# Kernel tuning notes

Hardware: AMD Instinct MI355X
Metric: run time of the kernel (lower is better)

## Reference

```python
import jax, jax.numpy as jnp
import numpy as np

D = 1024
H = 16
HD = D // H
FF = 4 * D
LN_EPS = 1e-5


def _layernorm(x, w, b):
    mu = jnp.mean(x, axis=-1, keepdims=True)
    var = jnp.mean(jnp.square(x - mu), axis=-1, keepdims=True)
    return (x - mu) * jax.lax.rsqrt(var + LN_EPS) * w + b


def setup_inputs() -> dict:
    key = jax.random.key(0)
    ks = jax.random.split(key, 12)
    s = 0.02
    return {
        "x": jax.random.normal(ks[0], (8, 1024, D), jnp.float32),
        "c": jax.random.normal(ks[1], (8, D), jnp.float32),
        "ln1_w": jnp.ones((D,), jnp.float32),
        "ln1_b": jnp.zeros((D,), jnp.float32),
        "ln2_w": jnp.ones((D,), jnp.float32),
        "ln2_b": jnp.zeros((D,), jnp.float32),
        "ada_w": jax.random.normal(ks[2], (D, 6 * D), jnp.float32) * s,
        "ada_b": jnp.zeros((6 * D,), jnp.float32),
        "qkv_w": jax.random.normal(ks[3], (D, 3 * D), jnp.float32) * s,
        "qkv_b": jnp.zeros((3 * D,), jnp.float32),
        "proj_w": jax.random.normal(ks[4], (D, D), jnp.float32) * s,
        "proj_b": jnp.zeros((D,), jnp.float32),
        "fc1_w": jax.random.normal(ks[5], (D, FF), jnp.float32) * s,
        "fc1_b": jnp.zeros((FF,), jnp.float32),
        "fc2_w": jax.random.normal(ks[6], (FF, D), jnp.float32) * s,
        "fc2_b": jnp.zeros((D,), jnp.float32),
    }


def reference(x, c, ln1_w, ln1_b, ln2_w, ln2_b, ada_w, ada_b,
              qkv_w, qkv_b, proj_w, proj_b, fc1_w, fc1_b, fc2_w, fc2_b):
    B, L, _ = x.shape
    # adaLN modulation: SiLU(c) @ W -> 6 chunks of (B, D)
    ssg = jax.nn.silu(c) @ ada_w + ada_b
    msa_shift, msa_scale, msa_gate, mlp_shift, mlp_scale, mlp_gate = jnp.split(ssg, 6, axis=-1)

    def modulate(h, shift, scale):
        return h * (1.0 + scale[:, None, :]) + shift[:, None, :]

    # ---- attention branch ----
    h = modulate(_layernorm(x, ln1_w, ln1_b), msa_shift, msa_scale)
    qkv = h @ qkv_w + qkv_b                      # (B, L, 3D)
    q, k, v = jnp.split(qkv, 3, axis=-1)
    q = q.reshape(B, L, H, HD).transpose(0, 2, 1, 3)   # (B, H, L, HD)
    k = k.reshape(B, L, H, HD).transpose(0, 2, 1, 3)
    v = v.reshape(B, L, H, HD).transpose(0, 2, 1, 3)
    scores = jnp.einsum("bhqd,bhkd->bhqk", q, k) / jnp.sqrt(jnp.float32(HD))
    attn = jax.nn.softmax(scores, axis=-1)
    a = jnp.einsum("bhqk,bhkd->bhqd", attn, v)   # (B, H, L, HD)
    a = a.transpose(0, 2, 1, 3).reshape(B, L, D)
    a = a @ proj_w + proj_b
    x = x + msa_gate[:, None, :] * a

    # ---- MLP branch ----
    h = modulate(_layernorm(x, ln2_w, ln2_b), mlp_shift, mlp_scale)
    h = jax.nn.gelu(h @ fc1_w + fc1_b, approximate=True)
    h = h @ fc2_w + fc2_b
    x = x + mlp_gate[:, None, :] * h
    return x
```

## Files before the change

kernel.cpp:

```cpp
#include <hip/hip_runtime.h>
#include <math.h>

#define DMODEL 1024
#define SIXD   6144
#define NHEAD  16
#define HEADD  64
#define LSEQ   1024
#define NBATCH 8
#define MROWS  8192

typedef unsigned short ushort_t;
typedef __attribute__((ext_vector_type(8))) short bf16x8;
typedef __attribute__((ext_vector_type(4))) float f32x4;

__device__ __forceinline__ unsigned short f2bf(float f) {
  unsigned int u = __float_as_uint(f);
  u += 0x7fff + ((u >> 16) & 1);
  return (unsigned short)(u >> 16);
}

__device__ __forceinline__ void gload_lds16(const void* g, void* l) {
  __builtin_amdgcn_global_load_lds(
      (const __attribute__((address_space(1))) unsigned int*)g,
      (__attribute__((address_space(3))) unsigned int*)l, 16, 0, 0);
}

__global__ void tcast_kernel(const float* __restrict__ W, ushort_t* __restrict__ WT,
                             int K, int N) {
  __shared__ float tile[32][33];
  int tx = threadIdx.x & 31, ty = threadIdx.x >> 5;
  int n0 = blockIdx.x * 32, k0 = blockIdx.y * 32;
#pragma unroll
  for (int r = 0; r < 4; ++r)
    tile[ty + 8*r][tx] = W[(size_t)(k0 + ty + 8*r) * N + n0 + tx];
  __syncthreads();
#pragma unroll
  for (int r = 0; r < 4; ++r)
    WT[(size_t)(n0 + ty + 8*r) * K + k0 + tx] = f2bf(tile[tx][ty + 8*r]);
}

__global__ __launch_bounds__(256) void vtrans_kernel(
    const ushort_t* __restrict__ qkvb, ushort_t* __restrict__ vT) {
  __shared__ ushort_t tile[128][66];
  int bh = blockIdx.x;
  int kt = blockIdx.y;
  int b = bh >> 4, h = bh & 15;
  int tid = threadIdx.x;
#pragma unroll
  for (int i = 0; i < 4; ++i) {
    int flat = tid + 256 * i;
    int r = flat >> 3, c8 = flat & 7;
    bf16x8 v = *(const bf16x8*)((const short*)qkvb +
        (size_t)(b * LSEQ + kt * 128 + r) * 3072 + 2048 + h * 64 + c8 * 8);
#pragma unroll
    for (int j = 0; j < 8; ++j) tile[r][c8 * 8 + j] = (ushort_t)v[j];
  }
  __syncthreads();
#pragma unroll
  for (int i = 0; i < 4; ++i) {
    int d = i * 16 + (tid >> 4);
    int kc = tid & 15;
    bf16x8 ov;
#pragma unroll
    for (int j = 0; j < 8; ++j) ov[j] = (short)tile[kc * 8 + j][d];
    *(bf16x8*)((short*)vT + (size_t)(bh * 64 + d) * 1024 + kt * 128 + kc * 8) = ov;
  }
}

__global__ void ada_kernel(const float* __restrict__ c, const float* __restrict__ ada_w,
                           const float* __restrict__ ada_b, float* __restrict__ ssg) {
  __shared__ float s[DMODEL];
  int b = blockIdx.y;
  int j = blockIdx.x * 256 + threadIdx.x;
  for (int i = threadIdx.x; i < DMODEL; i += 256) {
    float v = c[b * DMODEL + i];
    s[i] = v / (1.0f + __expf(-v));
  }
  __syncthreads();
  float acc = ada_b[j];
#pragma unroll 8
  for (int k = 0; k < DMODEL; ++k)
    acc = fmaf(s[k], ada_w[(size_t)k * SIXD + j], acc);
  ssg[b * SIXD + j] = acc;
}

__global__ __launch_bounds__(256) void ln_mod_kernel(
    const float* __restrict__ xin, const float* __restrict__ lw,
    const float* __restrict__ lb, const float* __restrict__ ssg,
    int shift_off, int scale_off, ushort_t* __restrict__ outB) {
  int row = blockIdx.x;
  int b = row >> 10;
  int tid = threadIdx.x;
  float4 v = ((const float4*)xin)[(size_t)row * 256 + tid];
  float sum = v.x + v.y + v.z + v.w;
  float sq  = v.x*v.x + v.y*v.y + v.z*v.z + v.w*v.w;
#pragma unroll
  for (int m = 32; m; m >>= 1) { sum += __shfl_xor(sum, m); sq += __shfl_xor(sq, m); }
  __shared__ float rbuf[8];
  int w = tid >> 6, lane = tid & 63;
  if (lane == 0) { rbuf[w] = sum; rbuf[4 + w] = sq; }
  __syncthreads();
  sum = rbuf[0] + rbuf[1] + rbuf[2] + rbuf[3];
  sq  = rbuf[4] + rbuf[5] + rbuf[6] + rbuf[7];
  float mu  = sum * (1.0f / 1024.0f);
  float var = sq * (1.0f / 1024.0f) - mu * mu;
  float rs  = rsqrtf(var + 1e-5f);
  const float* sg = ssg + b * SIXD;
  float vv[4] = {v.x, v.y, v.z, v.w};
  ushort4 pk;
  unsigned short* pks = (unsigned short*)&pk;
#pragma unroll
  for (int j = 0; j < 4; ++j) {
    int d = tid * 4 + j;
    float h = (vv[j] - mu) * rs * lw[d] + lb[d];
    h = h * (1.0f + sg[scale_off + d]) + sg[shift_off + d];
    pks[j] = f2bf(h);
  }
  ((ushort4*)outB)[(size_t)row * 256 + tid] = pk;
}

template <int EPI>
__global__ __launch_bounds__(256, 2) void gemm_kernel(
    const ushort_t* __restrict__ A, const ushort_t* __restrict__ BT,
    const float* __restrict__ bias, const float* __restrict__ ssg,
    const float* resid, float* outF, ushort_t* __restrict__ outB,
    int N, int K, int gate_off, int gxs) {
  __shared__ __align__(16) char SM[65536];
  int tid = threadIdx.x, lane = tid & 63, w = tid >> 6;
  int l15 = lane & 15, g = lane >> 4;
  int orig = blockIdx.x;
  int xcd = orig & 7;
  int idx = orig >> 3;
  int bxi = idx & ((1 << gxs) - 1);
  int byl = (idx >> gxs) & 7;
  int bxg = idx >> (gxs + 3);
  int bx = (bxg << gxs) + bxi;
  int by = (xcd << 3) + byl;
  int m0 = by * 128, n0 = bx * 128;
  int wrow = (w >> 1) * 64, wcol = (w & 1) * 64;
  f32x4 zero = {0.f, 0.f, 0.f, 0.f};
  f32x4 acc[4][4];
#pragma unroll
  for (int i = 0; i < 4; ++i)
#pragma unroll
    for (int j = 0; j < 4; ++j) acc[i][j] = zero;

  const char* asrc[4];
  const char* bsrc[4];
#pragma unroll
  for (int ch = 0; ch < 4; ++ch) {
    int flat = ch * 4096 + tid * 16;
    int row = flat >> 7;
    int colb = (flat & 127) ^ ((row & 7) << 4);
    asrc[ch] = (const char*)A  + ((size_t)(m0 + row) * K) * 2 + colb;
    bsrc[ch] = (const char*)BT + ((size_t)(n0 + row) * K) * 2 + colb;
  }

  int T = K >> 6;
#pragma unroll
  for (int ch = 0; ch < 4; ++ch)
    gload_lds16(asrc[ch], SM + ch * 4096 + tid * 16);
#pragma unroll
  for (int ch = 0; ch < 4; ++ch)
    gload_lds16(bsrc[ch], SM + 16384 + ch * 4096 + tid * 16);

  for (int t = 0; t < T; ++t) {
    if (t + 1 < T) {
      char* base = SM + ((t + 1) & 1) * 32768;
      size_t ko = (size_t)(t + 1) * 128;
#pragma unroll
      for (int ch = 0; ch < 4; ++ch)
        gload_lds16(asrc[ch] + ko, base + ch * 4096 + tid * 16);
#pragma unroll
      for (int ch = 0; ch < 4; ++ch)
        gload_lds16(bsrc[ch] + ko, base + 16384 + ch * 4096 + tid * 16);
      asm volatile("s_waitcnt vmcnt(8)" ::: "memory");
    } else {
      asm volatile("s_waitcnt vmcnt(0)" ::: "memory");
    }
    asm volatile("s_barrier" ::: "memory");
    const char* ab = SM + (t & 1) * 32768;
    const char* bb = ab + 16384;
#pragma unroll
    for (int kk = 0; kk < 2; ++kk) {
      bf16x8 af[4], bfr[4];
#pragma unroll
      for (int i = 0; i < 4; ++i) {
        int ar = wrow + i * 16 + l15;
        af[i]  = *(const bf16x8*)(ab + ar * 128 + ((kk * 64 + g * 16) ^ ((ar & 7) << 4)));
        int br = wcol + i * 16 + l15;
        bfr[i] = *(const bf16x8*)(bb + br * 128 + ((kk * 64 + g * 16) ^ ((br & 7) << 4)));
      }
#pragma unroll
      for (int i = 0; i < 4; ++i)
#pragma unroll
        for (int j = 0; j < 4; ++j)
          acc[i][j] = __builtin_amdgcn_mfma_f32_16x16x32_bf16(af[i], bfr[j], acc[i][j], 0, 0, 0);
    }
    asm volatile("s_barrier" ::: "memory");
  }
#pragma unroll
  for (int i = 0; i < 4; ++i)
#pragma unroll
    for (int j = 0; j < 4; ++j)
#pragma unroll
      for (int r = 0; r < 4; ++r) {
        int grow = m0 + wrow + i * 16 + g * 4 + r;
        int gcol = n0 + wcol + j * 16 + l15;
        float v = acc[i][j][r] + bias[gcol];
        if (EPI == 0) {
          outB[(size_t)grow * N + gcol] = f2bf(v);
        } else if (EPI == 1 || EPI == 3) {
          int bb2 = grow >> 10;
          float gate = ssg[bb2 * SIXD + gate_off + gcol];
          size_t idx2 = (size_t)grow * N + gcol;
          outF[idx2] = resid[idx2] + gate * v;
        } else {
          float u = v;
          float t2 = 0.7978845608028654f * (u + 0.044715f * u * u * u);
          float e = __expf(2.0f * t2);
          float th = 1.0f - 2.0f / (e + 1.0f);
          outB[(size_t)grow * N + gcol] = f2bf(0.5f * u * (1.0f + th));
        }
      }
}

__global__ __launch_bounds__(256, 2) void attn_kernel(
    const ushort_t* __restrict__ qkv,
    const ushort_t* __restrict__ vT,
    ushort_t* __restrict__ aout) {
  __shared__ __align__(16) char SM[33024];
  float* lbuf = (float*)(SM + 32768);
  int tid = threadIdx.x, lane = tid & 63, w = tid >> 6;
  int l15 = lane & 15, g = lane >> 4;
  int qt = blockIdx.x, bh = blockIdx.y;
  int b = bh >> 4, h = bh & 15;
  const float sc = 0.18033688f;

  bf16x8 aq[2];
  {
    int qrow = qt * 64 + w * 16 + l15;
    const short* qp = (const short*)qkv + (size_t)(b * LSEQ + qrow) * 3072 + h * 64 + g * 8;
    aq[0] = *(const bf16x8*)qp;
    aq[1] = *(const bf16x8*)(qp + 32);
#pragma unroll
    for (int ks = 0; ks < 2; ++ks) {
      union { bf16x8 v; unsigned short u[8]; } qi, qo;
      qi.v = aq[ks];
#pragma unroll
      for (int j = 0; j < 8; j += 2) {
        float lo = __uint_as_float((unsigned)qi.u[j] << 16) * sc;
        float hi = __uint_as_float((unsigned)qi.u[j + 1] << 16) * sc;
        unsigned pkd;
        asm("v_cvt_pk_bf16_f32 %0, %1, %2" : "=v"(pkd) : "v"(lo), "v"(hi));
        qo.u[j] = (unsigned short)(pkd & 0xffff);
        qo.u[j + 1] = (unsigned short)(pkd >> 16);
      }
      aq[ks] = qo.v;
    }
  }

  const char* ksrc[2];
  const char* vsrc[2];
#pragma unroll
  for (int p = 0; p < 2; ++p) {
    int flat = p * 4096 + w * 1024 + lane * 16;
    int row = flat >> 7;
    int colb = (flat & 127) ^ ((row & 7) << 4);
    ksrc[p] = (const char*)qkv + ((size_t)(b * LSEQ + row) * 3072 + 1024 + h * 64) * 2 + colb;
    vsrc[p] = (const char*)vT + ((size_t)(bh * 64 + row) * 1024) * 2 + colb;
  }

  f32x4 zero = {0.f, 0.f, 0.f, 0.f};
  f32x4 o[4] = {zero, zero, zero, zero};
  float lrow = 0.f;

#pragma unroll
  for (int p = 0; p < 2; ++p) {
    gload_lds16(ksrc[p], SM + p * 4096 + w * 1024);
    gload_lds16(vsrc[p], SM + 16384 + p * 4096 + w * 1024);
  }
  __syncthreads();

  for (int t = 0; t < 16; ++t) {
    int cur = t & 1;
    if (t < 15) {
      size_t koff = (size_t)(t + 1) * (64 * 3072 * 2);
      size_t voff = (size_t)(t + 1) * 128;
#pragma unroll
      for (int p = 0; p < 2; ++p) {
        gload_lds16(ksrc[p] + koff, SM + (cur ^ 1) * 8192 + p * 4096 + w * 1024);
        gload_lds16(vsrc[p] + voff, SM + 16384 + (cur ^ 1) * 8192 + p * 4096 + w * 1024);
      }
    }
    f32x4 s4[4] = {zero, zero, zero, zero};
    __builtin_amdgcn_s_setprio(1);
#pragma unroll
    for (int c = 0; c < 4; ++c)
#pragma unroll
      for (int ks = 0; ks < 2; ++ks) {
        int key = c * 16 + l15;
        bf16x8 ak = *(const bf16x8*)(SM + cur * 8192 + key * 128 +
                                     ((ks * 64 + g * 16) ^ ((key & 7) << 4)));
        s4[c] = __builtin_amdgcn_mfma_f32_16x16x32_bf16(ak, aq[ks], s4[c], 0, 0, 0);
      }
    __builtin_amdgcn_s_setprio(0);
    float p16[16], sump = 0.f;
#pragma unroll
    for (int c = 0; c < 4; ++c)
#pragma unroll
      for (int r = 0; r < 4; ++r) {
        float p = exp2f(s4[c][r]);
        p16[c * 4 + r] = p;
        sump += p;
      }
    sump += __shfl_xor(sump, 16);
    sump += __shfl_xor(sump, 32);
    lrow += sump;
    unsigned pk[8];
#pragma unroll
    for (int c = 0; c < 4; ++c)
#pragma unroll
      for (int m = 0; m < 2; ++m)
        asm("v_cvt_pk_bf16_f32 %0, %1, %2"
            : "=v"(pk[c * 2 + m]) : "v"(p16[c * 4 + 2 * m]), "v"(p16[c * 4 + 2 * m + 1]));
    unsigned pa[2][4];
    int gl = (g & 1) * 2;
#pragma unroll
    for (int kb = 0; kb < 2; ++kb)
#pragma unroll
      for (int wv = 0; wv < 4; ++wv) {
        int srcl = l15 + (gl + (wv >> 1)) * 16;
        unsigned vA = (unsigned)__shfl((int)pk[kb * 4 + (wv & 1)], srcl);
        unsigned vB = (unsigned)__shfl((int)pk[kb * 4 + 2 + (wv & 1)], srcl);
        pa[kb][wv] = (g >> 1) ? vB : vA;
      }
    union PU { unsigned u[4]; bf16x8 v; };
    PU pu0, pu1;
#pragma unroll
    for (int i = 0; i < 4; ++i) { pu0.u[i] = pa[0][i]; pu1.u[i] = pa[1][i]; }
    __builtin_amdgcn_s_setprio(1);
#pragma unroll
    for (int kb = 0; kb < 2; ++kb)
#pragma unroll
      for (int nb = 0; nb < 4; ++nb) {
        int d = nb * 16 + l15;
        bf16x8 bv = *(const bf16x8*)(SM + 16384 + cur * 8192 + d * 128 +
                                     ((kb * 64 + g * 16) ^ ((d & 7) << 4)));
        o[nb] = __builtin_amdgcn_mfma_f32_16x16x32_bf16(kb ? pu1.v : pu0.v, bv, o[nb], 0, 0, 0);
      }
    __builtin_amdgcn_s_setprio(0);
    __syncthreads();
  }
  if (lane < 16) lbuf[w * 16 + lane] = 1.0f / lrow;
  f32x4 rl = *(const f32x4*)&lbuf[w * 16 + g * 4];
#pragma unroll
  for (int nb = 0; nb < 4; ++nb)
#pragma unroll
    for (int r = 0; r < 4; ++r) {
      int qrow = qt * 64 + w * 16 + g * 4 + r;
      aout[(size_t)(b * LSEQ + qrow) * 1024 + h * 64 + nb * 16 + l15] =
          f2bf(o[nb][r] * rl[r]);
    }
}

extern "C" void kernel_launch(void* const* d_in, const int* in_sizes, int n_in,
                              void* d_out, int out_size, void* d_ws, size_t ws_size,
                              hipStream_t stream) {
  const float* x      = (const float*)d_in[0];
  const float* c      = (const float*)d_in[1];
  const float* ln1_w  = (const float*)d_in[2];
  const float* ln1_b  = (const float*)d_in[3];
  const float* ln2_w  = (const float*)d_in[4];
  const float* ln2_b  = (const float*)d_in[5];
  const float* ada_w  = (const float*)d_in[6];
  const float* ada_b  = (const float*)d_in[7];
  const float* qkv_w  = (const float*)d_in[8];
  const float* qkv_b  = (const float*)d_in[9];
  const float* proj_w = (const float*)d_in[10];
  const float* proj_b = (const float*)d_in[11];
  const float* fc1_w  = (const float*)d_in[12];
  const float* fc1_b  = (const float*)d_in[13];
  const float* fc2_w  = (const float*)d_in[14];
  const float* fc2_b  = (const float*)d_in[15];
  float* out = (float*)d_out;
  char* ws = (char*)d_ws;

  ushort_t* qkvT  = (ushort_t*)(ws + 0);
  ushort_t* projT = (ushort_t*)(ws + 6291456);
  ushort_t* fc1T  = (ushort_t*)(ws + 8388608);
  ushort_t* fc2T  = (ushort_t*)(ws + 16777216);
  float*    ssg   = (float*)(ws + 25165824);
  ushort_t* hbuf  = (ushort_t*)(ws + 25362432);
  ushort_t* abuf  = hbuf;
  ushort_t* qkvb  = (ushort_t*)(ws + 42139648);
  ushort_t* vTb   = (ushort_t*)(ws + 92471296);
  if (ws_size < (size_t)109248512) return;

  tcast_kernel<<<dim3(96, 32),  256, 0, stream>>>(qkv_w,  qkvT, 1024, 3072);
  tcast_kernel<<<dim3(32, 32),  256, 0, stream>>>(proj_w, projT, 1024, 1024);
  tcast_kernel<<<dim3(128, 32), 256, 0, stream>>>(fc1_w,  fc1T, 1024, 4096);
  tcast_kernel<<<dim3(32, 128), 256, 0, stream>>>(fc2_w,  fc2T, 4096, 1024);
  ada_kernel<<<dim3(24, 8), 256, 0, stream>>>(c, ada_w, ada_b, ssg);

  ln_mod_kernel<<<8192, 256, 0, stream>>>(x, ln1_w, ln1_b, ssg, 0, 1024, hbuf);
  gemm_kernel<0><<<1536, 256, 0, stream>>>(hbuf, qkvT, qkv_b, nullptr,
                                           nullptr, nullptr, qkvb, 3072, 1024, 0, 2);
  vtrans_kernel<<<dim3(128, 8), 256, 0, stream>>>(qkvb, vTb);
  attn_kernel<<<dim3(16, 128), 256, 0, stream>>>(qkvb, vTb, abuf);
  gemm_kernel<1><<<512, 256, 0, stream>>>(abuf, projT, proj_b, ssg,
                                          x, out, nullptr, 1024, 1024, 2048, 2);
  ln_mod_kernel<<<8192, 256, 0, stream>>>(out, ln2_w, ln2_b, ssg, 3072, 4096, hbuf);
  gemm_kernel<2><<<2048, 256, 0, stream>>>(hbuf, fc1T, fc1_b, nullptr,
                                           nullptr, nullptr, qkvb, 4096, 1024, 0, 2);
  gemm_kernel<3><<<512, 256, 0, stream>>>(qkvb, fc2T, fc2_b, ssg,
                                          out, out, nullptr, 1024, 4096, 5120, 3);
}
```

Before: 419.3 us.

## Load attention K/V fragments straight from global memory instead of LDS staging

The attention kernel drops its double-buffered LDS staging of K and V tiles, along with the barriers around it. Each wave now reads its K and V MFMA operand fragments directly from global memory into registers, and the final row normalisation uses shuffles instead of an LDS buffer. This removes LDS traffic and block-wide synchronisation and frees shared memory for occupancy. The cost is that all four waves fetch the same K/V tiles redundantly, with no explicit prefetch overlap, and more registers are used. A trailing integer argument of the final fc2 GEMM launch also changes from 3 to 1.

Result: slower. 571.8 us (+36.4%).

```diff
diff --git a/kernel.cpp b/kernel.cpp
--- a/kernel.cpp
+++ b/kernel.cpp
@@ -229,8 +229,6 @@
     const ushort_t* __restrict__ qkv,
     const ushort_t* __restrict__ vT,
     ushort_t* __restrict__ aout) {
-  __shared__ __align__(16) char SM[33024];
-  float* lbuf = (float*)(SM + 32768);
   int tid = threadIdx.x, lane = tid & 63, w = tid >> 6;
   int l15 = lane & 15, g = lane >> 4;
   int qt = blockIdx.x, bh = blockIdx.y;
@@ -260,50 +258,34 @@
     }
   }
 
-  const char* ksrc[2];
-  const char* vsrc[2];
-#pragma unroll
-  for (int p = 0; p < 2; ++p) {
-    int flat = p * 4096 + w * 1024 + lane * 16;
-    int row = flat >> 7;
-    int colb = (flat & 127) ^ ((row & 7) << 4);
-    ksrc[p] = (const char*)qkv + ((size_t)(b * LSEQ + row) * 3072 + 1024 + h * 64) * 2 + colb;
-    vsrc[p] = (const char*)vT + ((size_t)(bh * 64 + row) * 1024) * 2 + colb;
-  }
+  const short* kp = (const short*)qkv + (size_t)(b * LSEQ) * 3072 + 1024 + h * 64 + g * 8;
+  const short* vp = (const short*)vT + (size_t)(bh * 64) * 1024 + g * 8;
 
   f32x4 zero = {0.f, 0.f, 0.f, 0.f};
   f32x4 o[4] = {zero, zero, zero, zero};
   float lrow = 0.f;
 
-#pragma unroll
-  for (int p = 0; p < 2; ++p) {
-    gload_lds16(ksrc[p], SM + p * 4096 + w * 1024);
-    gload_lds16(vsrc[p], SM + 16384 + p * 4096 + w * 1024);
-  }
-  __syncthreads();
-
   for (int t = 0; t < 16; ++t) {
-    int cur = t & 1;
-    if (t < 15) {
-      size_t koff = (size_t)(t + 1) * (64 * 3072 * 2);
-      size_t voff = (size_t)(t + 1) * 128;
-#pragma unroll
-      for (int p = 0; p < 2; ++p) {
-        gload_lds16(ksrc[p] + koff, SM + (cur ^ 1) * 8192 + p * 4096 + w * 1024);
-        gload_lds16(vsrc[p] + voff, SM + 16384 + (cur ^ 1) * 8192 + p * 4096 + w * 1024);
-      }
-    }
+    int kv0 = t * 64;
+    bf16x8 kf[4][2];
+#pragma unroll
+    for (int c = 0; c < 4; ++c)
+#pragma unroll
+      for (int ks = 0; ks < 2; ++ks)
+        kf[c][ks] = *(const bf16x8*)(kp + (size_t)(kv0 + c * 16 + l15) * 3072 + ks * 32);
+    bf16x8 vf[2][4];
+#pragma unroll
+    for (int kb = 0; kb < 2; ++kb)
+#pragma unroll
+      for (int nb = 0; nb < 4; ++nb)
+        vf[kb][nb] = *(const bf16x8*)(vp + (size_t)(nb * 16 + l15) * 1024 + kv0 + kb * 32);
     f32x4 s4[4] = {zero, zero, zero, zero};
     __builtin_amdgcn_s_setprio(1);
 #pragma unroll
     for (int c = 0; c < 4; ++c)
 #pragma unroll
-      for (int ks = 0; ks < 2; ++ks) {
-        int key = c * 16 + l15;
-        bf16x8 ak = *(const bf16x8*)(SM + cur * 8192 + key * 128 +
-                                     ((ks * 64 + g * 16) ^ ((key & 7) << 4)));
-        s4[c] = __builtin_amdgcn_mfma_f32_16x16x32_bf16(ak, aq[ks], s4[c], 0, 0, 0);
-      }
+      for (int ks = 0; ks < 2; ++ks)
+        s4[c] = __builtin_amdgcn_mfma_f32_16x16x32_bf16(kf[c][ks], aq[ks], s4[c], 0, 0, 0);
     __builtin_amdgcn_s_setprio(0);
     float p16[16], sump = 0.f;
 #pragma unroll
@@ -343,24 +325,22 @@
 #pragma unroll
     for (int kb = 0; kb < 2; ++kb)
 #pragma unroll
-      for (int nb = 0; nb < 4; ++nb) {
-        int d = nb * 16 + l15;
-        bf16x8 bv = *(const bf16x8*)(SM + 16384 + cur * 8192 + d * 128 +
-                                     ((kb * 64 + g * 16) ^ ((d & 7) << 4)));
-        o[nb] = __builtin_amdgcn_mfma_f32_16x16x32_bf16(kb ? pu1.v : pu0.v, bv, o[nb], 0, 0, 0);
-      }
+      for (int nb = 0; nb < 4; ++nb)
+        o[nb] = __builtin_amdgcn_mfma_f32_16x16x32_bf16(kb ? pu1.v : pu0.v, vf[kb][nb], o[nb], 0, 0, 0);
     __builtin_amdgcn_s_setprio(0);
-    __syncthreads();
-  }
-  if (lane < 16) lbuf[w * 16 + lane] = 1.0f / lrow;
-  f32x4 rl = *(const f32x4*)&lbuf[w * 16 + g * 4];
+  }
+  float inv = 1.0f / lrow;
+  float rlr[4];
+#pragma unroll
+  for (int r = 0; r < 4; ++r)
+    rlr[r] = __shfl(inv, (lane & 48) + g * 4 + r);
 #pragma unroll
   for (int nb = 0; nb < 4; ++nb)
 #pragma unroll
     for (int r = 0; r < 4; ++r) {
       int qrow = qt * 64 + w * 16 + g * 4 + r;
       aout[(size_t)(b * LSEQ + qrow) * 1024 + h * 64 + nb * 16 + l15] =
-          f2bf(o[nb][r] * rl[r]);
+          f2bf(o[nb][r] * rlr[r]);
     }
 }
 
@@ -414,5 +394,5 @@
   gemm_kernel<2><<<2048, 256, 0, stream>>>(hbuf, fc1T, fc1_b, nullptr,
                                            nullptr, nullptr, qkvb, 4096, 1024, 0, 2);
   gemm_kernel<3><<<512, 256, 0, stream>>>(qkvb, fc2T, fc2_b, ssg,
-                                          out, out, nullptr, 1024, 4096, 5120, 3);
-}
+                                          out, out, nullptr, 1024, 4096, 5120, 1);
+}
```
